# Performance work log

Measured on AMD Instinct MI355X. Metric: run time of the kernel, lower is better.

Reference implementation:

```python
import jax, jax.numpy as jnp
import numpy as np

DIN = 1024
DIM = 1024
NUM_HEADS = 16
HEAD_DIM = DIM // NUM_HEADS
SEQ_LEN = 2048
BATCH = 2


def setup_inputs() -> dict:
    key = jax.random.key(0)
    ks = jax.random.split(key, 5)
    s = 0.02
    x = jax.random.normal(ks[0], (BATCH, SEQ_LEN, DIN), dtype=jnp.float32)
    # torch nn.Linear weights are (out_features, in_features)
    wq = jax.random.normal(ks[1], (DIM, DIN), dtype=jnp.float32) * s
    wk = jax.random.normal(ks[2], (DIM, DIN), dtype=jnp.float32) * s
    wv = jax.random.normal(ks[3], (DIM, DIN), dtype=jnp.float32) * s
    wo = jax.random.normal(ks[4], (DIM, DIM), dtype=jnp.float32) * s
    return {"x": x, "wq": wq, "wk": wk, "wv": wv, "wo": wo}


def reference(x, wq, wk, wv, wo):
    bs, seq_len, _ = x.shape
    # project and split heads: [b, h, s, d]
    def split(z):
        return z.reshape(bs, seq_len, NUM_HEADS, HEAD_DIM).transpose(0, 2, 1, 3)
    q = split(x @ wq.T)
    k = split(x @ wk.T)
    v = split(x @ wv.T)
    # raw scores, causal mask applied BEFORE the 1/sqrt(d) scaling (as in source;
    # -inf is invariant to positive scaling so math matches standard causal attn)
    att = jnp.einsum('bhqd,bhkd->bhqk', q, k)
    causal = jnp.triu(jnp.ones((seq_len, seq_len), dtype=bool), k=1)
    att = jnp.where(causal, -jnp.inf, att)
    att = jax.nn.softmax(att / jnp.sqrt(jnp.float32(HEAD_DIM)), axis=-1)
    ctx = jnp.einsum('bhqk,bhkd->bhqd', att, v)
    ctx = ctx.transpose(0, 2, 1, 3).reshape(bs, seq_len, DIM)
    return ctx @ wo.T
```

## Files before the change

### kernel.cpp

```cpp
#include <hip/hip_runtime.h>
#include <stdint.h>

#define DIN 1024
#define DIMM 1024
#define NH 16
#define HD 64
#define SEQ 2048
#define BATCH 2
#define MTOT (BATCH*SEQ)
#define LDP 72
#define SCALE 0.125f

typedef __bf16 bf16;
typedef __bf16 bf16x8 __attribute__((ext_vector_type(8)));
typedef __bf16 bf16x4 __attribute__((ext_vector_type(4)));
typedef float f32x4 __attribute__((ext_vector_type(4)));

__device__ __forceinline__ void async16(bf16* lds, const bf16* g) {
  __builtin_amdgcn_global_load_lds(
      (const __attribute__((address_space(1))) void*)g,
      (__attribute__((address_space(3))) void*)lds, 16, 0, 0);
}

__global__ __launch_bounds__(256) void convert_all(const float* __restrict__ x,
                                                   const float* __restrict__ wq,
                                                   const float* __restrict__ wk,
                                                   const float* __restrict__ wv,
                                                   const float* __restrict__ wo,
                                                   bf16* __restrict__ xb,
                                                   bf16* __restrict__ Wb) {
  const int t = blockIdx.x * 256 + threadIdx.x;
#pragma unroll
  for (int i = 0; i < 4; ++i) {
    const int c = t + i * 262144;
    const float* src;
    bf16* dst;
    if (c < 524288) {
      src = x + (size_t)c * 8;
      dst = xb + (size_t)c * 8;
    } else {
      const int cw = c - 524288;
      const int w = cw >> 17;
      const int off = (cw & 131071) * 8;
      const float* wp = (w == 0) ? wq : (w == 1) ? wk : (w == 2) ? wv : wo;
      src = wp + off;
      dst = Wb + (size_t)w * 1048576 + off;
    }
    f32x4 a = *(const f32x4*)src;
    f32x4 b = *(const f32x4*)(src + 4);
    bf16x8 r;
    r[0] = (bf16)a[0]; r[1] = (bf16)a[1]; r[2] = (bf16)a[2]; r[3] = (bf16)a[3];
    r[4] = (bf16)b[0]; r[5] = (bf16)b[1]; r[6] = (bf16)b[2]; r[7] = (bf16)b[3];
    *(bf16x8*)dst = r;
  }
}

__device__ __forceinline__ void mm128_core(const bf16* __restrict__ A,
                                           const bf16* __restrict__ B,
                                           int K, int mbase, int nbase,
                                           bf16* As, bf16* Bs,
                                           f32x4 acc[4][4]) {
  const int tid  = threadIdx.x;
  const int lane = tid & 63;
  const int wave = tid >> 6;
  const int lrow = lane & 15;
  const int quad = lane >> 4;
  const int wr = (wave >> 1) * 64;
  const int wc = (wave & 1) * 64;
  const int srow = tid >> 3;
  const int scol = (tid & 7) * 8;
  const int sx   = (((tid & 7) ^ (srow & 7))) * 8;

  for (int k0 = 0; k0 < K; k0 += 64) {
#pragma unroll
    for (int i = 0; i < 4; ++i) {
      async16(&As[(i * 32 + srow) * 64 + scol],
              &A[(size_t)(mbase + i * 32 + srow) * K + k0 + sx]);
      async16(&Bs[(i * 32 + srow) * 64 + scol],
              &B[(size_t)(nbase + i * 32 + srow) * K + k0 + sx]);
    }
    __syncthreads();
#pragma unroll
    for (int h = 0; h < 2; ++h) {
      const int cx = ((h * 4 + quad) ^ (lrow & 7)) * 8;
      bf16x8 af[4], bfr[4];
#pragma unroll
      for (int i = 0; i < 4; ++i) {
        af[i]  = *(const bf16x8*)&As[(wr + i * 16 + lrow) * 64 + cx];
        bfr[i] = *(const bf16x8*)&Bs[(wc + i * 16 + lrow) * 64 + cx];
      }
#pragma unroll
      for (int mt = 0; mt < 4; ++mt)
#pragma unroll
        for (int nt = 0; nt < 4; ++nt)
          acc[mt][nt] = __builtin_amdgcn_mfma_f32_16x16x32_bf16(af[mt], bfr[nt], acc[mt][nt], 0, 0, 0);
    }
    __syncthreads();
  }
}

__global__ __launch_bounds__(256) void qkv_gemm(const bf16* __restrict__ A,
                                                const bf16* __restrict__ B,
                                                bf16* __restrict__ Q,
                                                bf16* __restrict__ Kb,
                                                bf16* __restrict__ Vt) {
  __shared__ bf16 As[128 * 64];
  __shared__ bf16 Bs[128 * 64];
  const int lane = threadIdx.x & 63;
  const int wave = threadIdx.x >> 6;
  const int lrow = lane & 15;
  const int quad = lane >> 4;
  const int wr = (wave >> 1) * 64;
  const int wc = (wave & 1) * 64;
  const int mbase = blockIdx.y * 128;
  const int nbase = blockIdx.x * 128;

  f32x4 acc[4][4] = {};
  mm128_core(A, B, DIN, mbase, nbase, As, Bs, acc);

#pragma unroll
  for (int mt = 0; mt < 4; ++mt) {
    const int m0 = mbase + wr + mt * 16 + quad * 4;
#pragma unroll
    for (int nt = 0; nt < 4; ++nt) {
      const int n16 = nbase + wc + nt * 16;
      const int n = n16 + lrow;
      if (n16 < 1024) {
#pragma unroll
        for (int rr = 0; rr < 4; ++rr)
          Q[(size_t)(m0 + rr) * 1024 + n] = (bf16)acc[mt][nt][rr];
      } else if (n16 < 2048) {
#pragma unroll
        for (int rr = 0; rr < 4; ++rr)
          Kb[(size_t)(m0 + rr) * 1024 + (n - 1024)] = (bf16)acc[mt][nt][rr];
      } else {
        const int nn = n - 2048;
        const int row = ((m0 >> 11) * 16 + (nn >> 6)) * 64 + (nn & 63);
        bf16x4 ov;
#pragma unroll
        for (int rr = 0; rr < 4; ++rr) ov[rr] = (bf16)acc[mt][nt][rr];
        *(bf16x4*)&Vt[(size_t)row * SEQ + (m0 & 2047)] = ov;
      }
    }
  }
}

__global__ __launch_bounds__(256) void proj_gemm(const bf16* __restrict__ A,
                                                 const bf16* __restrict__ B,
                                                 float* __restrict__ C) {
  __shared__ bf16 As[128 * 64];
  __shared__ bf16 Bs[128 * 64];
  const int lane = threadIdx.x & 63;
  const int wave = threadIdx.x >> 6;
  const int lrow = lane & 15;
  const int quad = lane >> 4;
  const int wr = (wave >> 1) * 64;
  const int wc = (wave & 1) * 64;
  const int mbase = blockIdx.y * 128;
  const int nbase = blockIdx.x * 128;

  f32x4 acc[4][4] = {};
  mm128_core(A, B, DIMM, mbase, nbase, As, Bs, acc);

#pragma unroll
  for (int mt = 0; mt < 4; ++mt) {
    const int m0 = mbase + wr + mt * 16 + quad * 4;
#pragma unroll
    for (int nt = 0; nt < 4; ++nt) {
      const int n = nbase + wc + nt * 16 + lrow;
#pragma unroll
      for (int rr = 0; rr < 4; ++rr)
        C[(size_t)(m0 + rr) * 1024 + n] = acc[mt][nt][rr];
    }
  }
}

__global__ __launch_bounds__(512, 4) void attn(const bf16* __restrict__ Q,
                                               const bf16* __restrict__ K,
                                               const bf16* __restrict__ Vt,
                                               bf16* __restrict__ O) {
  __shared__ bf16 Ks[2][64 * 64];
  __shared__ bf16 Vts[2][64 * 64];
  __shared__ bf16 Plds[8][16 * LDP];
  const int tid  = threadIdx.x;
  const int wave = tid >> 6;
  const int lane = tid & 63;
  const int lrow = lane & 15;
  const int quad = lane >> 4;
  const int bh = blockIdx.x & 31;
  const int g  = blockIdx.x >> 5;
  const int qc = (g < 8) ? g : 23 - g;
  const int b  = bh >> 4;
  const int h  = bh & 15;
  const int qw = qc * 128 + wave * 16;
  const int ntiles = 2 * qc + 2;

  const bf16* Qh  = Q  + (size_t)(b * SEQ) * DIMM + h * HD;
  const bf16* Kh  = K  + (size_t)(b * SEQ) * DIMM + h * HD;
  const bf16* Vth = Vt + (size_t)bh * 64 * SEQ;
  bf16* Pw = Plds[wave];

  const int srow = tid >> 3;
  const int scol = (tid & 7) * 8;
  const int sx   = ((tid & 7) ^ (srow & 7)) * 8;
  const int cx0 = ((0 + quad) ^ (lrow & 7)) * 8;
  const int cx1 = ((4 + quad) ^ (lrow & 7)) * 8;

  bf16x8 qf0 = *(const bf16x8*)&Qh[(size_t)(qw + lrow) * DIMM + quad * 8];
  bf16x8 qf1 = *(const bf16x8*)&Qh[(size_t)(qw + lrow) * DIMM + 32 + quad * 8];

  async16(&Ks[0][srow * 64 + scol],  &Kh[(size_t)srow * DIMM + sx]);
  async16(&Vts[0][srow * 64 + scol], &Vth[(size_t)srow * SEQ + sx]);
  __syncthreads();

  float m_i = -1e30f, l_i = 0.f;
  f32x4 o_acc[4] = {};
  int cur = 0;

  for (int kt = 0; kt < ntiles; ++kt) {
    const int kbase = kt * 64;
    if (kt + 1 < ntiles) {
      const int nb = kbase + 64;
      async16(&Ks[cur ^ 1][srow * 64 + scol],  &Kh[(size_t)(nb + srow) * DIMM + sx]);
      async16(&Vts[cur ^ 1][srow * 64 + scol], &Vth[(size_t)srow * SEQ + nb + sx]);
    }
    if (kbase <= qw + 15) {
      const bf16* Kc = Ks[cur];
      const bf16* Vc = Vts[cur];
      f32x4 s[4] = {};
#pragma unroll
      for (int gg = 0; gg < 4; ++gg) {
        bf16x8 kf0 = *(const bf16x8*)&Kc[(gg * 16 + lrow) * 64 + cx0];
        bf16x8 kf1 = *(const bf16x8*)&Kc[(gg * 16 + lrow) * 64 + cx1];
        s[gg] = __builtin_amdgcn_mfma_f32_16x16x32_bf16(kf0, qf0, s[gg], 0, 0, 0);
        s[gg] = __builtin_amdgcn_mfma_f32_16x16x32_bf16(kf1, qf1, s[gg], 0, 0, 0);
      }
      if (kbase + 63 > qw) {
        const int qrow = qw + lrow;
#pragma unroll
        for (int gg = 0; gg < 4; ++gg)
#pragma unroll
          for (int r = 0; r < 4; ++r)
            s[gg][r] = (kbase + gg * 16 + quad * 4 + r > qrow) ? -1e30f : s[gg][r];
      }
      float pm = s[0][0];
#pragma unroll
      for (int gg = 0; gg < 4; ++gg)
#pragma unroll
        for (int r = 0; r < 4; ++r) pm = fmaxf(pm, s[gg][r]);
      pm = fmaxf(pm, __shfl_xor(pm, 16));
      pm = fmaxf(pm, __shfl_xor(pm, 32));
      const float mn = fmaxf(m_i, pm);
      const float al = __expf((m_i - mn) * SCALE);
      float sum = 0.f;
#pragma unroll
      for (int gg = 0; gg < 4; ++gg) {
        bf16x4 pk;
#pragma unroll
        for (int r = 0; r < 4; ++r) {
          const float p = __expf((s[gg][r] - mn) * SCALE);
          sum += p;
          pk[r] = (bf16)p;
        }
        *(bf16x4*)&Pw[lrow * LDP + gg * 16 + quad * 4] = pk;
      }
      sum += __shfl_xor(sum, 16);
      sum += __shfl_xor(sum, 32);
      l_i = l_i * al + sum;
      m_i = mn;
#pragma unroll
      for (int dt = 0; dt < 4; ++dt)
#pragma unroll
        for (int r = 0; r < 4; ++r)
          o_acc[dt][r] *= al;
      bf16x8 vf[8];
#pragma unroll
      for (int dt = 0; dt < 4; ++dt) {
        vf[2 * dt]     = *(const bf16x8*)&Vc[(dt * 16 + lrow) * 64 + cx0];
        vf[2 * dt + 1] = *(const bf16x8*)&Vc[(dt * 16 + lrow) * 64 + cx1];
      }
      bf16x8 pf0 = *(const bf16x8*)&Pw[lrow * LDP + quad * 8];
      bf16x8 pf1 = *(const bf16x8*)&Pw[lrow * LDP + 32 + quad * 8];
#pragma unroll
      for (int dt = 0; dt < 4; ++dt) {
        o_acc[dt] = __builtin_amdgcn_mfma_f32_16x16x32_bf16(vf[2 * dt],     pf0, o_acc[dt], 0, 0, 0);
        o_acc[dt] = __builtin_amdgcn_mfma_f32_16x16x32_bf16(vf[2 * dt + 1], pf1, o_acc[dt], 0, 0, 0);
      }
    }
    __syncthreads();
    cur ^= 1;
  }

  const float rl = __builtin_amdgcn_rcpf(l_i);
  bf16* Ob = O + (size_t)(b * SEQ + qw + lrow) * DIMM + h * HD;
#pragma unroll
  for (int dt = 0; dt < 4; ++dt) {
    bf16x4 ov;
#pragma unroll
    for (int r = 0; r < 4; ++r)
      ov[r] = (bf16)(o_acc[dt][r] * rl);
    *(bf16x4*)&Ob[dt * 16 + quad * 4] = ov;
  }
}

extern "C" void kernel_launch(void* const* d_in, const int* in_sizes, int n_in,
                              void* d_out, int out_size, void* d_ws, size_t ws_size,
                              hipStream_t stream) {
  const float* x  = (const float*)d_in[0];
  const float* wq = (const float*)d_in[1];
  const float* wk = (const float*)d_in[2];
  const float* wv = (const float*)d_in[3];
  const float* wo = (const float*)d_in[4];

  const size_t M4 = (size_t)MTOT * DIMM;
  bf16* xb  = (bf16*)d_ws;
  bf16* Wb  = xb + M4;
  bf16* Q   = Wb + M4;
  bf16* Kb  = Q + M4;
  bf16* Vt  = Kb + M4;
  bf16* CTX = xb;
  float* out = (float*)d_out;

  convert_all<<<dim3(1024), dim3(256), 0, stream>>>(x, wq, wk, wv, wo, xb, Wb);
  qkv_gemm<<<dim3(3072 / 128, MTOT / 128), dim3(256), 0, stream>>>(xb, Wb, Q, Kb, Vt);
  attn<<<dim3(BATCH * NH * (SEQ / 128)), dim3(512), 0, stream>>>(Q, Kb, Vt, CTX);
  proj_gemm<<<dim3(1024 / 128, MTOT / 128), dim3(256), 0, stream>>>(CTX, Wb + 3 * 1048576, out);
}
```

Measured before the change: 192.8 us.

## Fuse fp32-to-bf16 conversion into GEMM loads, shrink attention and proj tiles

Drops the separate conversion kernel. The QKV and output-projection GEMMs now read fp32 x and weights directly and convert them to bf16 while staging into LDS, using synchronous loads in place of async LDS loads for the converted operands. Attention blocks go from 128 query rows with 8 waves to 64 rows with 4 waves, with a four-way balanced query-chunk ordering and masking applied only on the last tile. The output-projection tile narrows to 128x64 for more blocks. This removes a launch and a round trip for x and weights, but the GEMMs re-read and re-convert fp32 data once per tile and lose async copy.

```diff
diff --git a/kernel.cpp b/kernel.cpp
--- a/kernel.cpp
+++ b/kernel.cpp
@@ -1,5 +1,6 @@
 #include <hip/hip_runtime.h>
 #include <stdint.h>
+#include <type_traits>
 
 #define DIN 1024
 #define DIMM 1024
@@ -22,44 +23,29 @@
       (__attribute__((address_space(3))) void*)lds, 16, 0, 0);
 }
 
-__global__ __launch_bounds__(256) void convert_all(const float* __restrict__ x,
-                                                   const float* __restrict__ wq,
-                                                   const float* __restrict__ wk,
-                                                   const float* __restrict__ wv,
-                                                   const float* __restrict__ wo,
-                                                   bf16* __restrict__ xb,
-                                                   bf16* __restrict__ Wb) {
-  const int t = blockIdx.x * 256 + threadIdx.x;
-#pragma unroll
-  for (int i = 0; i < 4; ++i) {
-    const int c = t + i * 262144;
-    const float* src;
-    bf16* dst;
-    if (c < 524288) {
-      src = x + (size_t)c * 8;
-      dst = xb + (size_t)c * 8;
-    } else {
-      const int cw = c - 524288;
-      const int w = cw >> 17;
-      const int off = (cw & 131071) * 8;
-      const float* wp = (w == 0) ? wq : (w == 1) ? wk : (w == 2) ? wv : wo;
-      src = wp + off;
-      dst = Wb + (size_t)w * 1048576 + off;
-    }
-    f32x4 a = *(const f32x4*)src;
-    f32x4 b = *(const f32x4*)(src + 4);
+template<typename T>
+__device__ __forceinline__ bf16x8 ld8bf16(const T* __restrict__ p) {
+  if constexpr (std::is_same<T, float>::value) {
+    const f32x4* q = (const f32x4*)p;
+    f32x4 a = q[0], b = q[1];
     bf16x8 r;
     r[0] = (bf16)a[0]; r[1] = (bf16)a[1]; r[2] = (bf16)a[2]; r[3] = (bf16)a[3];
     r[4] = (bf16)b[0]; r[5] = (bf16)b[1]; r[6] = (bf16)b[2]; r[7] = (bf16)b[3];
-    *(bf16x8*)dst = r;
-  }
-}
-
-__device__ __forceinline__ void mm128_core(const bf16* __restrict__ A,
-                                           const bf16* __restrict__ B,
-                                           int K, int mbase, int nbase,
-                                           bf16* As, bf16* Bs,
-                                           f32x4 acc[4][4]) {
+    return r;
+  } else {
+    return *(const bf16x8*)p;
+  }
+}
+
+__global__ __launch_bounds__(256) void qkv_gemm(const float* __restrict__ x,
+                                                const float* __restrict__ wq,
+                                                const float* __restrict__ wk,
+                                                const float* __restrict__ wv,
+                                                bf16* __restrict__ Q,
+                                                bf16* __restrict__ Kb,
+                                                bf16* __restrict__ Vt) {
+  __shared__ bf16 As[128 * 64];
+  __shared__ bf16 Bs[128 * 64];
   const int tid  = threadIdx.x;
   const int lane = tid & 63;
   const int wave = tid >> 6;
@@ -67,17 +53,24 @@
   const int quad = lane >> 4;
   const int wr = (wave >> 1) * 64;
   const int wc = (wave & 1) * 64;
+  const int mbase = blockIdx.y * 128;
+  const int nbase = blockIdx.x * 128;
   const int srow = tid >> 3;
   const int scol = (tid & 7) * 8;
-  const int sx   = (((tid & 7) ^ (srow & 7))) * 8;
-
-  for (int k0 = 0; k0 < K; k0 += 64) {
+  const int sx   = ((tid & 7) ^ (srow & 7)) * 8;
+
+  const float* W = (nbase < 1024) ? wq : (nbase < 2048) ? wk : wv;
+  const int nb2  = nbase & 1023;
+
+  f32x4 acc[4][4] = {};
+
+  for (int k0 = 0; k0 < DIN; k0 += 64) {
 #pragma unroll
     for (int i = 0; i < 4; ++i) {
-      async16(&As[(i * 32 + srow) * 64 + scol],
-              &A[(size_t)(mbase + i * 32 + srow) * K + k0 + sx]);
-      async16(&Bs[(i * 32 + srow) * 64 + scol],
-              &B[(size_t)(nbase + i * 32 + srow) * K + k0 + sx]);
+      *(bf16x8*)&As[(i * 32 + srow) * 64 + scol] =
+          ld8bf16(&x[(size_t)(mbase + i * 32 + srow) * DIN + k0 + sx]);
+      *(bf16x8*)&Bs[(i * 32 + srow) * 64 + scol] =
+          ld8bf16(&W[(size_t)(nb2 + i * 32 + srow) * DIN + k0 + sx]);
     }
     __syncthreads();
 #pragma unroll
@@ -97,26 +90,6 @@
     }
     __syncthreads();
   }
-}
-
-__global__ __launch_bounds__(256) void qkv_gemm(const bf16* __restrict__ A,
-                                                const bf16* __restrict__ B,
-                                                bf16* __restrict__ Q,
-                                                bf16* __restrict__ Kb,
-                                                bf16* __restrict__ Vt) {
-  __shared__ bf16 As[128 * 64];
-  __shared__ bf16 Bs[128 * 64];
-  const int lane = threadIdx.x & 63;
-  const int wave = threadIdx.x >> 6;
-  const int lrow = lane & 15;
-  const int quad = lane >> 4;
-  const int wr = (wave >> 1) * 64;
-  const int wc = (wave & 1) * 64;
-  const int mbase = blockIdx.y * 128;
-  const int nbase = blockIdx.x * 128;
-
-  f32x4 acc[4][4] = {};
-  mm128_core(A, B, DIN, mbase, nbase, As, Bs, acc);
 
 #pragma unroll
   for (int mt = 0; mt < 4; ++mt) {
@@ -146,27 +119,59 @@
 }
 
 __global__ __launch_bounds__(256) void proj_gemm(const bf16* __restrict__ A,
-                                                 const bf16* __restrict__ B,
+                                                 const float* __restrict__ W,
                                                  float* __restrict__ C) {
   __shared__ bf16 As[128 * 64];
-  __shared__ bf16 Bs[128 * 64];
-  const int lane = threadIdx.x & 63;
-  const int wave = threadIdx.x >> 6;
+  __shared__ bf16 Bs[64 * 64];
+  const int tid  = threadIdx.x;
+  const int lane = tid & 63;
+  const int wave = tid >> 6;
   const int lrow = lane & 15;
   const int quad = lane >> 4;
   const int wr = (wave >> 1) * 64;
-  const int wc = (wave & 1) * 64;
+  const int wc = (wave & 1) * 32;
   const int mbase = blockIdx.y * 128;
-  const int nbase = blockIdx.x * 128;
-
-  f32x4 acc[4][4] = {};
-  mm128_core(A, B, DIMM, mbase, nbase, As, Bs, acc);
+  const int nbase = blockIdx.x * 64;
+  const int srow = tid >> 3;
+  const int scol = (tid & 7) * 8;
+  const int sx   = ((tid & 7) ^ (srow & 7)) * 8;
+
+  f32x4 acc[4][2] = {};
+
+  for (int k0 = 0; k0 < DIMM; k0 += 64) {
+#pragma unroll
+    for (int i = 0; i < 4; ++i)
+      async16(&As[(i * 32 + srow) * 64 + scol],
+              &A[(size_t)(mbase + i * 32 + srow) * DIMM + k0 + sx]);
+#pragma unroll
+    for (int i = 0; i < 2; ++i)
+      *(bf16x8*)&Bs[(i * 32 + srow) * 64 + scol] =
+          ld8bf16(&W[(size_t)(nbase + i * 32 + srow) * DIMM + k0 + sx]);
+    __syncthreads();
+#pragma unroll
+    for (int h = 0; h < 2; ++h) {
+      const int cx = ((h * 4 + quad) ^ (lrow & 7)) * 8;
+      bf16x8 af[4], bfr[2];
+#pragma unroll
+      for (int i = 0; i < 4; ++i)
+        af[i] = *(const bf16x8*)&As[(wr + i * 16 + lrow) * 64 + cx];
+#pragma unroll
+      for (int i = 0; i < 2; ++i)
+        bfr[i] = *(const bf16x8*)&Bs[(wc + i * 16 + lrow) * 64 + cx];
+#pragma unroll
+      for (int mt = 0; mt < 4; ++mt)
+#pragma unroll
+        for (int nt = 0; nt < 2; ++nt)
+          acc[mt][nt] = __builtin_amdgcn_mfma_f32_16x16x32_bf16(af[mt], bfr[nt], acc[mt][nt], 0, 0, 0);
+    }
+    __syncthreads();
+  }
 
 #pragma unroll
   for (int mt = 0; mt < 4; ++mt) {
     const int m0 = mbase + wr + mt * 16 + quad * 4;
 #pragma unroll
-    for (int nt = 0; nt < 4; ++nt) {
+    for (int nt = 0; nt < 2; ++nt) {
       const int n = nbase + wc + nt * 16 + lrow;
 #pragma unroll
       for (int rr = 0; rr < 4; ++rr)
@@ -175,13 +180,13 @@
   }
 }
 
-__global__ __launch_bounds__(512, 4) void attn(const bf16* __restrict__ Q,
+__global__ __launch_bounds__(256, 4) void attn(const bf16* __restrict__ Q,
                                                const bf16* __restrict__ K,
                                                const bf16* __restrict__ Vt,
                                                bf16* __restrict__ O) {
   __shared__ bf16 Ks[2][64 * 64];
   __shared__ bf16 Vts[2][64 * 64];
-  __shared__ bf16 Plds[8][16 * LDP];
+  __shared__ bf16 Plds[4][16 * LDP];
   const int tid  = threadIdx.x;
   const int wave = tid >> 6;
   const int lane = tid & 63;
@@ -189,11 +194,12 @@
   const int quad = lane >> 4;
   const int bh = blockIdx.x & 31;
   const int g  = blockIdx.x >> 5;
-  const int qc = (g < 8) ? g : 23 - g;
+  const int j  = g >> 3, g0 = g & 7;
+  const int qc = (j == 0) ? g0 : (j == 1) ? 15 - g0 : (j == 2) ? 16 + g0 : 31 - g0;
   const int b  = bh >> 4;
   const int h  = bh & 15;
-  const int qw = qc * 128 + wave * 16;
-  const int ntiles = 2 * qc + 2;
+  const int qw = qc * 64 + wave * 16;
+  const int ntiles = qc + 1;
 
   const bf16* Qh  = Q  + (size_t)(b * SEQ) * DIMM + h * HD;
   const bf16* Kh  = K  + (size_t)(b * SEQ) * DIMM + h * HD;
@@ -209,8 +215,11 @@
   bf16x8 qf0 = *(const bf16x8*)&Qh[(size_t)(qw + lrow) * DIMM + quad * 8];
   bf16x8 qf1 = *(const bf16x8*)&Qh[(size_t)(qw + lrow) * DIMM + 32 + quad * 8];
 
-  async16(&Ks[0][srow * 64 + scol],  &Kh[(size_t)srow * DIMM + sx]);
-  async16(&Vts[0][srow * 64 + scol], &Vth[(size_t)srow * SEQ + sx]);
+#pragma unroll
+  for (int i = 0; i < 2; ++i) {
+    async16(&Ks[0][(i * 32 + srow) * 64 + scol],  &Kh[(size_t)(i * 32 + srow) * DIMM + sx]);
+    async16(&Vts[0][(i * 32 + srow) * 64 + scol], &Vth[(size_t)(i * 32 + srow) * SEQ + sx]);
+  }
   __syncthreads();
 
   float m_i = -1e30f, l_i = 0.f;
@@ -221,71 +230,74 @@
     const int kbase = kt * 64;
     if (kt + 1 < ntiles) {
       const int nb = kbase + 64;
-      async16(&Ks[cur ^ 1][srow * 64 + scol],  &Kh[(size_t)(nb + srow) * DIMM + sx]);
-      async16(&Vts[cur ^ 1][srow * 64 + scol], &Vth[(size_t)srow * SEQ + nb + sx]);
-    }
-    if (kbase <= qw + 15) {
-      const bf16* Kc = Ks[cur];
-      const bf16* Vc = Vts[cur];
-      f32x4 s[4] = {};
-#pragma unroll
-      for (int gg = 0; gg < 4; ++gg) {
-        bf16x8 kf0 = *(const bf16x8*)&Kc[(gg * 16 + lrow) * 64 + cx0];
-        bf16x8 kf1 = *(const bf16x8*)&Kc[(gg * 16 + lrow) * 64 + cx1];
-        s[gg] = __builtin_amdgcn_mfma_f32_16x16x32_bf16(kf0, qf0, s[gg], 0, 0, 0);
-        s[gg] = __builtin_amdgcn_mfma_f32_16x16x32_bf16(kf1, qf1, s[gg], 0, 0, 0);
+#pragma unroll
+      for (int i = 0; i < 2; ++i) {
+        async16(&Ks[cur ^ 1][(i * 32 + srow) * 64 + scol],
+                &Kh[(size_t)(nb + i * 32 + srow) * DIMM + sx]);
+        async16(&Vts[cur ^ 1][(i * 32 + srow) * 64 + scol],
+                &Vth[(size_t)(i * 32 + srow) * SEQ + nb + sx]);
       }
-      if (kbase + 63 > qw) {
-        const int qrow = qw + lrow;
-#pragma unroll
-        for (int gg = 0; gg < 4; ++gg)
-#pragma unroll
-          for (int r = 0; r < 4; ++r)
-            s[gg][r] = (kbase + gg * 16 + quad * 4 + r > qrow) ? -1e30f : s[gg][r];
+    }
+    const bf16* Kc = Ks[cur];
+    const bf16* Vc = Vts[cur];
+    f32x4 s[4] = {};
+#pragma unroll
+    for (int gg = 0; gg < 4; ++gg) {
+      bf16x8 kf0 = *(const bf16x8*)&Kc[(gg * 16 + lrow) * 64 + cx0];
+      bf16x8 kf1 = *(const bf16x8*)&Kc[(gg * 16 + lrow) * 64 + cx1];
+      s[gg] = __builtin_amdgcn_mfma_f32_16x16x32_bf16(kf0, qf0, s[gg], 0, 0, 0);
+      s[gg] = __builtin_amdgcn_mfma_f32_16x16x32_bf16(kf1, qf1, s[gg], 0, 0, 0);
+    }
+    if (kt == ntiles - 1) {
+      const int qrow = qw + lrow;
+#pragma unroll
+      for (int gg = 0; gg < 4; ++gg)
+#pragma unroll
+        for (int r = 0; r < 4; ++r)
+          s[gg][r] = (kbase + gg * 16 + quad * 4 + r > qrow) ? -1e30f : s[gg][r];
+    }
+    float pm = s[0][0];
+#pragma unroll
+    for (int gg = 0; gg < 4; ++gg)
+#pragma unroll
+      for (int r = 0; r < 4; ++r) pm = fmaxf(pm, s[gg][r]);
+    pm = fmaxf(pm, __shfl_xor(pm, 16));
+    pm = fmaxf(pm, __shfl_xor(pm, 32));
+    const float mn = fmaxf(m_i, pm);
+    const float al = __expf((m_i - mn) * SCALE);
+    float sum = 0.f;
+#pragma unroll
+    for (int gg = 0; gg < 4; ++gg) {
+      bf16x4 pk;
+#pragma unroll
+      for (int r = 0; r < 4; ++r) {
+        const float p = __expf((s[gg][r] - mn) * SCALE);
+        sum += p;
+        pk[r] = (bf16)p;
       }
-      float pm = s[0][0];
-#pragma unroll
-      for (int gg = 0; gg < 4; ++gg)
-#pragma unroll
-        for (int r = 0; r < 4; ++r) pm = fmaxf(pm, s[gg][r]);
-      pm = fmaxf(pm, __shfl_xor(pm, 16));
-      pm = fmaxf(pm, __shfl_xor(pm, 32));
-      const float mn = fmaxf(m_i, pm);
-      const float al = __expf((m_i - mn) * SCALE);
-      float sum = 0.f;
-#pragma unroll
-      for (int gg = 0; gg < 4; ++gg) {
-        bf16x4 pk;
-#pragma unroll
-        for (int r = 0; r < 4; ++r) {
-          const float p = __expf((s[gg][r] - mn) * SCALE);
-          sum += p;
-          pk[r] = (bf16)p;
-        }
-        *(bf16x4*)&Pw[lrow * LDP + gg * 16 + quad * 4] = pk;
-      }
-      sum += __shfl_xor(sum, 16);
-      sum += __shfl_xor(sum, 32);
-      l_i = l_i * al + sum;
-      m_i = mn;
-#pragma unroll
-      for (int dt = 0; dt < 4; ++dt)
-#pragma unroll
-        for (int r = 0; r < 4; ++r)
-          o_acc[dt][r] *= al;
-      bf16x8 vf[8];
-#pragma unroll
-      for (int dt = 0; dt < 4; ++dt) {
-        vf[2 * dt]     = *(const bf16x8*)&Vc[(dt * 16 + lrow) * 64 + cx0];
-        vf[2 * dt + 1] = *(const bf16x8*)&Vc[(dt * 16 + lrow) * 64 + cx1];
-      }
-      bf16x8 pf0 = *(const bf16x8*)&Pw[lrow * LDP + quad * 8];
-      bf16x8 pf1 = *(const bf16x8*)&Pw[lrow * LDP + 32 + quad * 8];
-#pragma unroll
-      for (int dt = 0; dt < 4; ++dt) {
-        o_acc[dt] = __builtin_amdgcn_mfma_f32_16x16x32_bf16(vf[2 * dt],     pf0, o_acc[dt], 0, 0, 0);
-        o_acc[dt] = __builtin_amdgcn_mfma_f32_16x16x32_bf16(vf[2 * dt + 1], pf1, o_acc[dt], 0, 0, 0);
-      }
+      *(bf16x4*)&Pw[lrow * LDP + gg * 16 + quad * 4] = pk;
+    }
+    sum += __shfl_xor(sum, 16);
+    sum += __shfl_xor(sum, 32);
+    l_i = l_i * al + sum;
+    m_i = mn;
+#pragma unroll
+    for (int dt = 0; dt < 4; ++dt)
+#pragma unroll
+      for (int r = 0; r < 4; ++r)
+        o_acc[dt][r] *= al;
+    bf16x8 vf[8];
+#pragma unroll
+    for (int dt = 0; dt < 4; ++dt) {
+      vf[2 * dt]     = *(const bf16x8*)&Vc[(dt * 16 + lrow) * 64 + cx0];
+      vf[2 * dt + 1] = *(const bf16x8*)&Vc[(dt * 16 + lrow) * 64 + cx1];
+    }
+    bf16x8 pf0 = *(const bf16x8*)&Pw[lrow * LDP + quad * 8];
+    bf16x8 pf1 = *(const bf16x8*)&Pw[lrow * LDP + 32 + quad * 8];
+#pragma unroll
+    for (int dt = 0; dt < 4; ++dt) {
+      o_acc[dt] = __builtin_amdgcn_mfma_f32_16x16x32_bf16(vf[2 * dt],     pf0, o_acc[dt], 0, 0, 0);
+      o_acc[dt] = __builtin_amdgcn_mfma_f32_16x16x32_bf16(vf[2 * dt + 1], pf1, o_acc[dt], 0, 0, 0);
     }
     __syncthreads();
     cur ^= 1;
@@ -313,16 +325,13 @@
   const float* wo = (const float*)d_in[4];
 
   const size_t M4 = (size_t)MTOT * DIMM;
-  bf16* xb  = (bf16*)d_ws;
-  bf16* Wb  = xb + M4;
-  bf16* Q   = Wb + M4;
+  bf16* Q   = (bf16*)d_ws;
   bf16* Kb  = Q + M4;
   bf16* Vt  = Kb + M4;
-  bf16* CTX = xb;
+  bf16* CTX = Vt + M4;
   float* out = (float*)d_out;
 
-  convert_all<<<dim3(1024), dim3(256), 0, stream>>>(x, wq, wk, wv, wo, xb, Wb);
-  qkv_gemm<<<dim3(3072 / 128, MTOT / 128), dim3(256), 0, stream>>>(xb, Wb, Q, Kb, Vt);
-  attn<<<dim3(BATCH * NH * (SEQ / 128)), dim3(512), 0, stream>>>(Q, Kb, Vt, CTX);
-  proj_gemm<<<dim3(1024 / 128, MTOT / 128), dim3(256), 0, stream>>>(CTX, Wb + 3 * 1048576, out);
-}
+  qkv_gemm<<<dim3(3072 / 128, MTOT / 128), dim3(256), 0, stream>>>(x, wq, wk, wv, Q, Kb, Vt);
+  attn<<<dim3(BATCH * NH * (SEQ / 64)), dim3(256), 0, stream>>>(Q, Kb, Vt, CTX);
+  proj_gemm<<<dim3(1024 / 64, MTOT / 128), dim3(256), 0, stream>>>(CTX, wo, out);
+}
```

Result: slower. 209.4 us (+8.6%).
